# Optimization experiments

Measured on AMD Instinct MI355X. Metric: run time of the kernel, lower is better.

The kernel has to match this reference:

```python
import jax, jax.numpy as jnp
import numpy as np
from jax import lax

EPS = 1e-8
ROUTINGS = 3


def squash(u, axis=-1):
    norm = jnp.linalg.norm(u, axis=axis, keepdims=True)
    scale = norm ** 2 / (1 + norm ** 2) / (norm + EPS)
    return scale * u


def conv2d(x, w, b, stride):
    y = lax.conv_general_dilated(x, w, window_strides=(stride, stride), padding='VALID',
                                 dimension_numbers=('NCHW', 'OIHW', 'NCHW'))
    return y + b[None, :, None, None]


def setup_inputs() -> dict:
    key = jax.random.key(0)
    ks = jax.random.split(key, 6)
    x = jax.random.normal(ks[0], (512, 1, 28, 28), dtype=jnp.float32)
    conv1_w = 0.1 * jax.random.normal(ks[1], (256, 1, 9, 9), dtype=jnp.float32)
    conv1_b = 0.1 * jax.random.normal(ks[2], (256,), dtype=jnp.float32)
    pc_w = 0.01 * jax.random.normal(ks[3], (256, 256, 9, 9), dtype=jnp.float32)
    pc_b = 0.01 * jax.random.normal(ks[4], (256,), dtype=jnp.float32)
    caps_w = 0.01 * jax.random.normal(ks[5], (10, 1152, 16, 8), dtype=jnp.float32)
    return {"x": x, "conv1_w": conv1_w, "conv1_b": conv1_b,
            "pc_w": pc_w, "pc_b": pc_b, "caps_w": caps_w}


def reference(x, conv1_w, conv1_b, pc_w, pc_b, caps_w):
    B = x.shape[0]
    # conv1 + relu: [B,1,28,28] -> [B,256,20,20]
    h = jax.nn.relu(conv2d(x, conv1_w, conv1_b, stride=1))
    # primary capsules: [B,256,20,20] -> [B,256,6,6] -> [B,1152,8], squash
    h = conv2d(h, pc_w, pc_b, stride=2)
    u = squash(h.reshape(B, 1152, 8))
    # votes: weight [O,I,Do,Di] x u [B,I,Di] -> x_hat [B,O,I,Do]
    x_hat = jnp.einsum('oidk,bik->boid', caps_w, u)
    x_hat_det = lax.stop_gradient(x_hat)
    b_logits = jnp.zeros((B, caps_w.shape[0], caps_w.shape[1]), dtype=x_hat.dtype)
    out_caps = None
    for i in range(ROUTINGS):
        c = jax.nn.softmax(b_logits, axis=1)  # softmax over output caps
        if i == ROUTINGS - 1:
            out_caps = squash(jnp.sum(c[..., None] * x_hat, axis=2))  # [B,O,Do]
        else:
            v = squash(jnp.sum(c[..., None] * x_hat_det, axis=2))  # [B,O,Do]
            b_logits = b_logits + jnp.einsum('bod,boid->boi', v, x_hat_det)
    length = jnp.linalg.norm(out_caps, axis=-1)  # [B,O]
    return length
```

## Files before the change

kernel.cpp:

```cpp
#include <hip/hip_runtime.h>
#include <hip/hip_bf16.h>
#include <hip/hip_fp16.h>
#include <math.h>

#define EPS 1e-8f

typedef __attribute__((ext_vector_type(8))) short bf16x8;
typedef __attribute__((ext_vector_type(8))) _Float16 f16x8;
typedef __attribute__((ext_vector_type(4))) float f32x4;
typedef __attribute__((ext_vector_type(16))) float f32x16;

__device__ static inline unsigned short f2bf(float f) {
    __hip_bfloat16 h = __float2bfloat16(f);
    return *reinterpret_cast<unsigned short*>(&h);
}
__device__ static inline unsigned short f2h(float f) {
    __half h = __float2half(f);
    return *reinterpret_cast<unsigned short*>(&h);
}

__device__ static inline void gld_lds16(const void* g, void* l) {
    __builtin_amdgcn_global_load_lds((const __attribute__((address_space(1))) void*)g,
                                     (__attribute__((address_space(3))) void*)l, 16, 0, 0);
}

__device__ static inline void h8tof(uint4 w, float* f) {
    float2 a = __half22float2(*(__half2*)&w.x);
    float2 b = __half22float2(*(__half2*)&w.y);
    float2 c = __half22float2(*(__half2*)&w.z);
    float2 d = __half22float2(*(__half2*)&w.w);
    f[0] = a.x; f[1] = a.y; f[2] = b.x; f[3] = b.y;
    f[4] = c.x; f[5] = c.y; f[6] = d.x; f[7] = d.y;
}

__global__ void k_prep(const float* __restrict__ x, unsigned short* __restrict__ xh,
                       const float* __restrict__ w1, unsigned short* __restrict__ wt1h,
                       const float* __restrict__ cw, __half* __restrict__ cwh) {
    int idx = blockIdx.x * 256 + threadIdx.x;
    if (idx < 401408) {
        xh[idx] = f2h(x[idx]);
    } else if (idx < 401408 + 24576) {
        int j = idx - 401408;
        int n = j / 96, k = j % 96;
        wt1h[j] = (k < 81) ? f2h(w1[n * 81 + k]) : (unsigned short)0;
    } else {
        int j = idx - 401408 - 24576;
        cwh[j] = __float2half(cw[j]);
    }
}

__global__ __launch_bounds__(256) void k_tw2(const float* __restrict__ pw,
                                             unsigned short* __restrict__ wt2t) {
    __shared__ unsigned short lds[20736];
    const int oc = blockIdx.x, t = threadIdx.x;
    const float* src = pw + (size_t)oc * 20736;
#pragma unroll
    for (int it = 0; it < 81; ++it) {
        int j = it * 256 + t;
        lds[j] = f2bf(src[j]);
    }
    __syncthreads();
    unsigned short* dst = wt2t + (size_t)oc * 20736;
#pragma unroll
    for (int it = 0; it < 81; ++it) {
        int j = it * 256 + t;
        int q = j >> 8, ic = j & 255;
        dst[j] = lds[ic * 81 + q];
    }
}

__global__ __launch_bounds__(256) void k_conv1(const unsigned short* __restrict__ xh,
                                               const unsigned short* __restrict__ wt1h,
                                               const float* __restrict__ b1,
                                               unsigned short* __restrict__ h1) {
    __shared__ unsigned short Asm[128 * 104];
    __shared__ unsigned short Bsm[128 * 104];
    const int tid = threadIdx.x;
    const int wave = tid >> 6, lane = tid & 63;
    const int ln15 = lane & 15, quad = lane >> 4;
    const int m0 = blockIdx.x * 128;
    const int n0 = blockIdx.y * 128;
    const int wm = (wave >> 1) * 64, wn = (wave & 1) * 64;

    for (int c = tid; c < 1536; c += 256) {
        int r = c / 12, ch = c % 12;
        uint4 v = *(const uint4*)(wt1h + (size_t)(n0 + r) * 96 + ch * 8);
        *(uint4*)(&Bsm[r * 104 + ch * 8]) = v;
    }
    for (int s = 0; s < 5; ++s) {
        int id = s * 256 + tid;
        if (id < 1152) {
            int m_l = id & 127, kh = id >> 7;
            int m = m0 + m_l;
            int b = m / 400, sp = m % 400;
            int oh = sp / 20, ow = sp % 20;
            const unsigned short* src = xh + b * 784 + (oh + kh) * 28 + ow;
            unsigned short* drow = &Asm[m_l * 104 + kh * 9];
#pragma unroll
            for (int w = 0; w < 9; ++w) drow[w] = src[w];
        }
    }
    for (int z = tid; z < 1920; z += 256) {
        int r = z / 15, kk = 81 + z % 15;
        Asm[r * 104 + kk] = 0;
    }
    __syncthreads();

    f32x4 acc[4][4];
#pragma unroll
    for (int i = 0; i < 4; ++i)
#pragma unroll
        for (int j = 0; j < 4; ++j) acc[i][j] = (f32x4)(0.f);

#pragma unroll
    for (int ks = 0; ks < 3; ++ks) {
        int k0 = (ks * 4 + quad) * 8;
        f16x8 af[4], bfr[4];
#pragma unroll
        for (int i = 0; i < 4; ++i)
            af[i] = *(const f16x8*)&Asm[(wm + i * 16 + ln15) * 104 + k0];
#pragma unroll
        for (int j = 0; j < 4; ++j)
            bfr[j] = *(const f16x8*)&Bsm[(wn + j * 16 + ln15) * 104 + k0];
#pragma unroll
        for (int i = 0; i < 4; ++i)
#pragma unroll
            for (int j = 0; j < 4; ++j)
                acc[i][j] = __builtin_amdgcn_mfma_f32_16x16x32_f16(
                    af[i], bfr[j], acc[i][j], 0, 0, 0);
    }

    float bias[4];
#pragma unroll
    for (int j = 0; j < 4; ++j) bias[j] = b1[n0 + wn + j * 16 + ln15];
#pragma unroll
    for (int i = 0; i < 4; ++i) {
#pragma unroll
        for (int r = 0; r < 4; ++r) {
            int m = m0 + wm + i * 16 + quad * 4 + r;
            unsigned short* dst = h1 + (size_t)m * 256 + n0 + wn;
#pragma unroll
            for (int j = 0; j < 4; ++j) {
                float v = acc[i][j][r] + bias[j];
                dst[j * 16 + ln15] = f2bf(v > 0.f ? v : 0.f);
            }
        }
    }
}

__global__ __launch_bounds__(256) void k_conv2(const unsigned short* __restrict__ h1,
                                               const unsigned short* __restrict__ wt2t,
                                               unsigned short* __restrict__ h2a) {
    __shared__ short Asm[128 * 64];
    __shared__ short Bsm[64 * 64];

    const int tid  = threadIdx.x;
    const int wave = tid >> 6, lane = tid & 63;
    const int ln31 = lane & 31, ln7 = lane & 7, khalf = lane >> 5;
    const int m0 = blockIdx.x * 128;
    const int n0 = blockIdx.y * 64;
    const int zz = blockIdx.z;
    const int kt0 = zz * 54;
    const int wm = wave * 32;

    const int cswz8 = ((lane & 7) ^ ((lane >> 3) & 7)) * 8;

    size_t aptr[4];
#pragma unroll
    for (int s = 0; s < 4; ++s) {
        int r = wave * 32 + (lane >> 3) + s * 8;
        int m = m0 + r;
        int b = m / 36, sp = m % 36;
        int oh = sp / 6, ow = sp % 6;
        aptr[s] = (size_t)((b * 20 + 2 * oh) * 20 + 2 * ow) * 256 + cswz8;
    }
    size_t bptr[2];
#pragma unroll
    for (int s = 0; s < 2; ++s) {
        int r = wave * 16 + (lane >> 3) + s * 8;
        bptr[s] = (size_t)(n0 + r) * 20736 + cswz8;
    }
    short* alds = &Asm[(wave * 32) * 64 + lane * 8];
    short* blds = &Bsm[(wave * 16) * 64 + lane * 8];

    f32x16 acc[2];
    acc[0] = (f32x16)(0.f);
    acc[1] = (f32x16)(0.f);

    int q0 = kt0 >> 2;
    int kh = q0 / 9, kw = q0 - kh * 9;
    int pix = (kh * 20 + kw) * 256;

    for (int kt = kt0; kt < kt0 + 54; ++kt) {
        size_t aoff = (size_t)pix + ((kt & 3) << 6);
        size_t boff = (size_t)kt << 6;
#pragma unroll
        for (int s = 0; s < 4; ++s)
            gld_lds16(h1 + aptr[s] + aoff, alds + s * 512);
#pragma unroll
        for (int s = 0; s < 2; ++s)
            gld_lds16(wt2t + bptr[s] + boff, blds + s * 512);
        __syncthreads();
#pragma unroll
        for (int ks = 0; ks < 4; ++ks) {
            int slot = ((ks << 1) + khalf) ^ ln7;
            bf16x8 af = *(const bf16x8*)&Asm[(wm + ln31) * 64 + slot * 8];
            bf16x8 b0 = *(const bf16x8*)&Bsm[(ln31) * 64 + slot * 8];
            bf16x8 b1v = *(const bf16x8*)&Bsm[(32 + ln31) * 64 + slot * 8];
            acc[0] = __builtin_amdgcn_mfma_f32_32x32x16_bf16(af, b0,  acc[0], 0, 0, 0);
            acc[1] = __builtin_amdgcn_mfma_f32_32x32x16_bf16(af, b1v, acc[1], 0, 0, 0);
        }
        __syncthreads();
        if ((kt & 3) == 3) {
            if (kw == 8) { kw = 0; ++kh; pix += 12 * 256; }
            else         { ++kw;       pix += 256; }
        }
    }

    unsigned short* zs = h2a + (size_t)zz * 4718592;
#pragma unroll
    for (int j = 0; j < 2; ++j) {
#pragma unroll
        for (int reg = 0; reg < 16; ++reg) {
            int row = (reg & 3) + 8 * (reg >> 2) + 4 * khalf;
            int m = m0 + wm + row;
            zs[(size_t)m * 256 + n0 + j * 32 + ln31] = f2h(acc[j][reg]);
        }
    }
}

__global__ __launch_bounds__(256) void k_squash(const unsigned short* __restrict__ h2a,
                                                const float* __restrict__ pb,
                                                unsigned short* __restrict__ u) {
    __shared__ float tile[36 * 260];
    const int tid = threadIdx.x;
    const int b = blockIdx.x;
    const unsigned short* base = h2a + (size_t)b * 9216;
    for (int idx = tid; idx < 1152; idx += 256) {
        int sp = idx >> 5, c8 = (idx & 31) * 8;
        float v[8];
#pragma unroll
        for (int e = 0; e < 8; ++e) v[e] = pb[c8 + e];
#pragma unroll
        for (int z = 0; z < 6; ++z) {
            uint4 w = *(const uint4*)(base + (size_t)z * 4718592 + sp * 256 + c8);
            float f[8];
            h8tof(w, f);
#pragma unroll
            for (int e = 0; e < 8; ++e) v[e] += f[e];
        }
#pragma unroll
        for (int e = 0; e < 8; ++e) tile[sp * 260 + c8 + e] = v[e];
    }
    __syncthreads();
    for (int i2 = tid; i2 < 1152; i2 += 256) {
        int f0 = i2 * 8;
        float val[8];
        float n2 = 0.f;
#pragma unroll
        for (int e = 0; e < 8; ++e) {
            int f = f0 + e;
            int c = f / 36, sp = f - c * 36;
            val[e] = tile[sp * 260 + c];
            n2 += val[e] * val[e];
        }
        float n = sqrtf(n2);
        float s = n2 / (1.f + n2) / (n + EPS);
        unsigned short o8[8];
#pragma unroll
        for (int e = 0; e < 8; ++e) o8[e] = f2h(val[e] * s);
        *(uint4*)(u + (size_t)b * 9216 + f0) = *(uint4*)o8;
    }
}

__global__ __launch_bounds__(256) void k_xhat(const unsigned short* __restrict__ u,
                                              const __half* __restrict__ cwh,
                                              __half* __restrict__ xhat,
                                              float* __restrict__ s0) {
    __shared__ float part[4][16];
    const int b = blockIdx.x, o = blockIdx.y;
    const int t = threadIdx.x;
    const uint4* ub = (const uint4*)(u + (size_t)b * 9216);
    float s_loc[16];
#pragma unroll
    for (int d = 0; d < 16; ++d) s_loc[d] = 0.f;

    for (int i = t; i < 1152; i += 256) {
        float ui[8];
        h8tof(ub[i], ui);
        const uint4* wp = (const uint4*)(cwh + ((size_t)(o * 1152 + i) << 7));
        unsigned short xv[16];
#pragma unroll
        for (int d = 0; d < 16; ++d) {
            float f[8];
            h8tof(wp[d], f);
            float xh = f[0] * ui[0] + f[1] * ui[1] + f[2] * ui[2] + f[3] * ui[3]
                     + f[4] * ui[4] + f[5] * ui[5] + f[6] * ui[6] + f[7] * ui[7];
            s_loc[d] += xh;
            xv[d] = f2h(xh);
        }
        __half* dst = xhat + ((size_t)((b * 10 + o) * 1152 + i)) * 16;
        *(uint4*)dst       = *(uint4*)xv;
        *(uint4*)(dst + 8) = *(uint4*)(xv + 8);
    }
#pragma unroll
    for (int off = 32; off > 0; off >>= 1)
#pragma unroll
        for (int d = 0; d < 16; ++d) s_loc[d] += __shfl_down(s_loc[d], off, 64);
    if ((t & 63) == 0) {
#pragma unroll
        for (int d = 0; d < 16; ++d) part[t >> 6][d] = s_loc[d];
    }
    __syncthreads();
    if (t < 16)
        s0[(b * 10 + o) * 16 + t] = part[0][t] + part[1][t] + part[2][t] + part[3][t];
}

__global__ __launch_bounds__(640) void k_routing(const __half* __restrict__ xhat,
                                                 const float* __restrict__ s0,
                                                 float* __restrict__ out) {
    __shared__ float dots[10][1152];
    __shared__ float sv[10][16];
    __shared__ float vsum[10][16];
    __shared__ float scale_sh[10];
    const int t = threadIdx.x;
    const int b = blockIdx.x;
    const int o = t >> 6, lane = t & 63;
    const __half* xb = xhat + ((size_t)(b * 10 + o) * 1152) * 16;

    if (t < 160) {
        int oo = t >> 4, d = t & 15;
        sv[oo][d] = 0.1f * s0[(b * 10 + oo) * 16 + d];
    }
    __syncthreads();
    if (t < 10) {
        float n2 = 0.f;
#pragma unroll
        for (int d = 0; d < 16; ++d) n2 += sv[t][d] * sv[t][d];
        float n = sqrtf(n2);
        scale_sh[t] = n2 / (1.f + n2) / (n + EPS);
    }
    __syncthreads();
    if (t < 160) vsum[t >> 4][t & 15] = sv[t >> 4][t & 15] * scale_sh[t >> 4];
    __syncthreads();

    for (int pass = 1; pass <= 2; ++pass) {
        float vs[16];
#pragma unroll
        for (int d = 0; d < 16; ++d) vs[d] = vsum[o][d];
        float s_loc[16];
#pragma unroll
        for (int d = 0; d < 16; ++d) s_loc[d] = 0.f;

        for (int g = 0; g < 6; ++g) {
            uint4 xq[3][2];
#pragma unroll
            for (int j = 0; j < 3; ++j) {
                int i = g * 192 + j * 64 + lane;
                const uint4* p = (const uint4*)(xb + (size_t)i * 16);
                xq[j][0] = p[0];
                xq[j][1] = p[1];
                float f0[8], f1[8];
                h8tof(xq[j][0], f0);
                h8tof(xq[j][1], f1);
                float dd = 0.f;
#pragma unroll
                for (int d = 0; d < 8; ++d) dd += vs[d] * f0[d] + vs[d + 8] * f1[d];
                dots[o][i] = dd;
            }
            __syncthreads();
            if (t < 192) {
                int i = g * 192 + t;
                float dv[10];
#pragma unroll
                for (int oo = 0; oo < 10; ++oo) dv[oo] = dots[oo][i];
                float mx = dv[0];
#pragma unroll
                for (int oo = 1; oo < 10; ++oo) mx = fmaxf(mx, dv[oo]);
                float se = 0.f;
#pragma unroll
                for (int oo = 0; oo < 10; ++oo) { dv[oo] = __expf(dv[oo] - mx); se += dv[oo]; }
                float si = 1.f / se;
#pragma unroll
                for (int oo = 0; oo < 10; ++oo) dots[oo][i] = dv[oo] * si;
            }
            __syncthreads();
#pragma unroll
            for (int j = 0; j < 3; ++j) {
                int i = g * 192 + j * 64 + lane;
                float c = dots[o][i];
                float f0[8], f1[8];
                h8tof(xq[j][0], f0);
                h8tof(xq[j][1], f1);
#pragma unroll
                for (int d = 0; d < 8; ++d) {
                    s_loc[d]     += c * f0[d];
                    s_loc[d + 8] += c * f1[d];
                }
            }
        }
#pragma unroll
        for (int off = 32; off > 0; off >>= 1)
#pragma unroll
            for (int d = 0; d < 16; ++d) s_loc[d] += __shfl_down(s_loc[d], off, 64);
        if (lane == 0) {
#pragma unroll
            for (int d = 0; d < 16; ++d) sv[o][d] = s_loc[d];
        }
        __syncthreads();
        if (pass == 1) {
            if (t < 10) {
                float n2 = 0.f;
#pragma unroll
                for (int d = 0; d < 16; ++d) n2 += sv[t][d] * sv[t][d];
                float n = sqrtf(n2);
                scale_sh[t] = n2 / (1.f + n2) / (n + EPS);
            }
            __syncthreads();
            if (t < 160) {
                int oo = t >> 4, d = t & 15;
                vsum[oo][d] += sv[oo][d] * scale_sh[oo];
            }
            __syncthreads();
        } else {
            if (t < 10) {
                float n2 = 0.f;
#pragma unroll
                for (int d = 0; d < 16; ++d) n2 += sv[t][d] * sv[t][d];
                float n = sqrtf(n2);
                out[b * 10 + t] = (n2 / (1.f + n2)) * (n / (n + EPS));
            }
        }
    }
}

extern "C" void kernel_launch(void* const* d_in, const int* in_sizes, int n_in,
                              void* d_out, int out_size, void* d_ws, size_t ws_size,
                              hipStream_t stream) {
    const float* x  = (const float*)d_in[0];
    const float* w1 = (const float*)d_in[1];
    const float* b1 = (const float*)d_in[2];
    const float* pw = (const float*)d_in[3];
    const float* pb = (const float*)d_in[4];
    const float* cw = (const float*)d_in[5];
    float* out = (float*)d_out;

    char* ws = (char*)d_ws;
    unsigned short* h1   = (unsigned short*)ws;
    unsigned short* h2a  = (unsigned short*)(ws + 104857600);
    unsigned short* wt2t = (unsigned short*)(ws + 161480704);
    __half*         xhat = (__half*)ws;
    unsigned short* u    = (unsigned short*)(ws + 188743680);
    __half*         cwh  = (__half*)(ws + 198180864);
    unsigned short* xh16 = (unsigned short*)(ws + 201129984);
    unsigned short* wt1h = (unsigned short*)(ws + 201932800);
    float*          s0   = (float*)(ws + 201981952);

    k_prep<<<7424, 256, 0, stream>>>(x, xh16, w1, wt1h, cw, cwh);
    k_tw2<<<256, 256, 0, stream>>>(pw, wt2t);
    k_conv1<<<dim3(1600, 2), 256, 0, stream>>>(xh16, wt1h, b1, h1);
    k_conv2<<<dim3(144, 4, 6), 256, 0, stream>>>(h1, wt2t, h2a);
    k_squash<<<512, 256, 0, stream>>>(h2a, pb, u);
    k_xhat<<<dim3(512, 10), 256, 0, stream>>>(u, cwh, xhat, s0);
    k_routing<<<512, 640, 0, stream>>>(xhat, s0, out);
}
```

Baseline: 625.6 us.

## Widen conv2 block tile to all 256 output channels with 2x4 MFMA per wave

The conv2 implicit GEMM block tile grows from 128x64 to 128x256, so each block covers every output channel, and the grid drops the N dimension. Each wave now computes a 64x128 sub-tile with 8 accumulators, which improves reuse of the A (activation) tile in LDS and stops reloading it four times across N blocks. The cost is 4x more B staging per block, more LDS (48KB), higher register pressure, and only 864 blocks, which lowers occupancy and parallelism.

Measured after the change: 708.2 us. 1.13x slower.

```diff
diff --git a/kernel.cpp b/kernel.cpp
--- a/kernel.cpp
+++ b/kernel.cpp
@@ -152,16 +152,16 @@
                                                const unsigned short* __restrict__ wt2t,
                                                unsigned short* __restrict__ h2a) {
     __shared__ short Asm[128 * 64];
-    __shared__ short Bsm[64 * 64];
+    __shared__ short Bsm[256 * 64];
 
     const int tid  = threadIdx.x;
     const int wave = tid >> 6, lane = tid & 63;
     const int ln31 = lane & 31, ln7 = lane & 7, khalf = lane >> 5;
     const int m0 = blockIdx.x * 128;
-    const int n0 = blockIdx.y * 64;
-    const int zz = blockIdx.z;
+    const int zz = blockIdx.y;
     const int kt0 = zz * 54;
-    const int wm = wave * 32;
+    const int wm = (wave >> 1) * 64;
+    const int wn = (wave & 1) * 128;
 
     const int cswz8 = ((lane & 7) ^ ((lane >> 3) & 7)) * 8;
 
@@ -174,18 +174,16 @@
         int oh = sp / 6, ow = sp % 6;
         aptr[s] = (size_t)((b * 20 + 2 * oh) * 20 + 2 * ow) * 256 + cswz8;
     }
-    size_t bptr[2];
-#pragma unroll
-    for (int s = 0; s < 2; ++s) {
-        int r = wave * 16 + (lane >> 3) + s * 8;
-        bptr[s] = (size_t)(n0 + r) * 20736 + cswz8;
-    }
+    const size_t bbase = (size_t)(wave * 64 + (lane >> 3)) * 20736 + cswz8;
+
     short* alds = &Asm[(wave * 32) * 64 + lane * 8];
-    short* blds = &Bsm[(wave * 16) * 64 + lane * 8];
-
-    f32x16 acc[2];
-    acc[0] = (f32x16)(0.f);
-    acc[1] = (f32x16)(0.f);
+    short* blds = &Bsm[(wave * 64) * 64 + lane * 8];
+
+    f32x16 acc[2][4];
+#pragma unroll
+    for (int i = 0; i < 2; ++i)
+#pragma unroll
+        for (int j = 0; j < 4; ++j) acc[i][j] = (f32x16)(0.f);
 
     int q0 = kt0 >> 2;
     int kh = q0 / 9, kw = q0 - kh * 9;
@@ -198,17 +196,25 @@
         for (int s = 0; s < 4; ++s)
             gld_lds16(h1 + aptr[s] + aoff, alds + s * 512);
 #pragma unroll
-        for (int s = 0; s < 2; ++s)
-            gld_lds16(wt2t + bptr[s] + boff, blds + s * 512);
+        for (int s = 0; s < 8; ++s)
+            gld_lds16(wt2t + bbase + (size_t)s * 8 * 20736 + boff, blds + s * 512);
         __syncthreads();
 #pragma unroll
         for (int ks = 0; ks < 4; ++ks) {
             int slot = ((ks << 1) + khalf) ^ ln7;
-            bf16x8 af = *(const bf16x8*)&Asm[(wm + ln31) * 64 + slot * 8];
-            bf16x8 b0 = *(const bf16x8*)&Bsm[(ln31) * 64 + slot * 8];
-            bf16x8 b1v = *(const bf16x8*)&Bsm[(32 + ln31) * 64 + slot * 8];
-            acc[0] = __builtin_amdgcn_mfma_f32_32x32x16_bf16(af, b0,  acc[0], 0, 0, 0);
-            acc[1] = __builtin_amdgcn_mfma_f32_32x32x16_bf16(af, b1v, acc[1], 0, 0, 0);
+            bf16x8 af[2], bfr[4];
+#pragma unroll
+            for (int i = 0; i < 2; ++i)
+                af[i] = *(const bf16x8*)&Asm[(wm + i * 32 + ln31) * 64 + slot * 8];
+#pragma unroll
+            for (int j = 0; j < 4; ++j)
+                bfr[j] = *(const bf16x8*)&Bsm[(wn + j * 32 + ln31) * 64 + slot * 8];
+#pragma unroll
+            for (int i = 0; i < 2; ++i)
+#pragma unroll
+                for (int j = 0; j < 4; ++j)
+                    acc[i][j] = __builtin_amdgcn_mfma_f32_32x32x16_bf16(
+                        af[i], bfr[j], acc[i][j], 0, 0, 0);
         }
         __syncthreads();
         if ((kt & 3) == 3) {
@@ -219,12 +225,15 @@
 
     unsigned short* zs = h2a + (size_t)zz * 4718592;
 #pragma unroll
-    for (int j = 0; j < 2; ++j) {
-#pragma unroll
-        for (int reg = 0; reg < 16; ++reg) {
-            int row = (reg & 3) + 8 * (reg >> 2) + 4 * khalf;
-            int m = m0 + wm + row;
-            zs[(size_t)m * 256 + n0 + j * 32 + ln31] = f2h(acc[j][reg]);
+    for (int i = 0; i < 2; ++i) {
+#pragma unroll
+        for (int j = 0; j < 4; ++j) {
+#pragma unroll
+            for (int reg = 0; reg < 16; ++reg) {
+                int row = (reg & 3) + 8 * (reg >> 2) + 4 * khalf;
+                int m = m0 + wm + i * 32 + row;
+                zs[(size_t)m * 256 + wn + j * 32 + ln31] = f2h(acc[i][j][reg]);
+            }
         }
     }
 }
@@ -459,7 +468,7 @@
     k_prep<<<7424, 256, 0, stream>>>(x, xh16, w1, wt1h, cw, cwh);
     k_tw2<<<256, 256, 0, stream>>>(pw, wt2t);
     k_conv1<<<dim3(1600, 2), 256, 0, stream>>>(xh16, wt1h, b1, h1);
-    k_conv2<<<dim3(144, 4, 6), 256, 0, stream>>>(h1, wt2t, h2a);
+    k_conv2<<<dim3(144, 6), 256, 0, stream>>>(h1, wt2t, h2a);
     k_squash<<<512, 256, 0, stream>>>(h2a, pb, u);
     k_xhat<<<dim3(512, 10), 256, 0, stream>>>(u, cwh, xhat, s0);
     k_routing<<<512, 640, 0, stream>>>(xhat, s0, out);
```
